# Kernel tuning notes

Measured on AMD Instinct MI355X. Metric: run time of the kernel, lower is better.

## Reference

```python
import jax, jax.numpy as jnp
import numpy as np

E = 16          # ensemble_size
S = 64          # state_size
A = 32          # action_size
R = 1           # reward_size
I = S + A       # combined input size
HS = 64         # SubModel_state hidden
HR = 32         # SubModel_reward hidden
B = 16384       # batch


def setup_inputs() -> dict:
    key = jax.random.key(0)
    ks = jax.random.split(key, 10)

    def init_lin(k, fan_in, shape):
        bound = 1.0 / np.sqrt(fan_in)
        return jax.random.uniform(k, shape, jnp.float32, -bound, bound)

    return {
        "state": jax.random.normal(ks[0], (B, S), jnp.float32),
        "action": jax.random.normal(ks[1], (B, A), jnp.float32),
        # stacked ensemble state-model weights (torch Linear stores [out,in]; we use [in,out])
        "W1": init_lin(ks[2], I, (E, I, HS)),
        "b1": init_lin(ks[3], I, (E, HS)),
        "W2": init_lin(ks[4], HS, (E, HS, S)),
        "b2": init_lin(ks[5], HS, (E, S)),
        # stacked ensemble reward-model weights
        "rW1": init_lin(ks[6], I, (E, I, HR)),
        "rb1": init_lin(ks[7], I, (E, HR)),
        "rW2": init_lin(ks[8], HR, (E, HR, R)),
        "rb2": init_lin(ks[9], HR, (E, R)),
    }


def reference(state, action, W1, b1, W2, b2, rW1, rb1, rW2, rb2):
    x = jnp.concatenate([state, action], axis=1)  # [B, I]
    # state models: Linear -> ReLU -> Linear, all ensemble members in one batched GEMM
    h = jax.nn.relu(jnp.einsum("bi,eih->ebh", x, W1) + b1[:, None, :])  # [E, B, HS]
    pred_states = jnp.einsum("ebh,ehs->ebs", h, W2) + b2[:, None, :]    # [E, B, S]
    # reward models: Linear -> ReLU -> Linear -> clamp(-100, 200)
    hr = jax.nn.relu(jnp.einsum("bi,eih->ebh", x, rW1) + rb1[:, None, :])  # [E, B, HR]
    pred_rewards = jnp.einsum("ebh,ehr->ebr", hr, rW2) + rb2[:, None, :]   # [E, B, R]
    pred_rewards = jnp.clip(pred_rewards, -100.0, 200.0)
    return (pred_states, pred_rewards)
```

## Files before the change

### kernel.cpp

```cpp
#include <hip/hip_runtime.h>
#include <hip/hip_bf16.h>
#include <cstdint>
#include <cstddef>

#define Bsz 16384
#define Esz 16
#define Ssz 64
#define Asz 32
#define Isz 96
#define HSz 64
#define HRz 32

#define NTM 256
#define CHUNK 512
#define NTILE 8

typedef __attribute__((ext_vector_type(8))) short bf16x8;
typedef __attribute__((ext_vector_type(4))) short short4v;
typedef __attribute__((ext_vector_type(4))) float f32x4;

static __device__ __forceinline__ short f2bf(float f) {
    __hip_bfloat16 b = __float2bfloat16(f);
    return *reinterpret_cast<short*>(&b);
}
static __device__ __forceinline__ float bf2f(short s) {
    union { uint32_t u; float f; } v; v.u = ((uint32_t)(uint16_t)s) << 16; return v.f;
}
static __device__ __forceinline__ bf16x8 pack8(float4 lo, float4 hi) {
    bf16x8 r;
    r[0] = f2bf(lo.x); r[1] = f2bf(lo.y); r[2] = f2bf(lo.z); r[3] = f2bf(lo.w);
    r[4] = f2bf(hi.x); r[5] = f2bf(hi.y); r[6] = f2bf(hi.z); r[7] = f2bf(hi.w);
    return r;
}

__global__ __launch_bounds__(NTM, 2)
void fused_all(const float* __restrict__ state, const float* __restrict__ action,
               const float* __restrict__ W1, const float* __restrict__ b1,
               const float* __restrict__ W2, const float* __restrict__ b2,
               const float* __restrict__ rW1, const float* __restrict__ rb1,
               const float* __restrict__ rW2, const float* __restrict__ rb2,
               float* __restrict__ outS, float* __restrict__ outR)
{
    __shared__ __align__(16) short HT[4][16][68];
    __shared__ __align__(16) float OT[4][16][72];

    const int bid = blockIdx.x;
    const int xcd = bid & 7;
    const int rem = bid >> 3;
    const int e   = rem & (Esz - 1);
    const int c0  = (xcd + 8 * (rem >> 4)) * CHUNK;

    const int w = threadIdx.x >> 6, lane = threadIdx.x & 63;
    const int lr = lane & 15, lg = lane >> 4;

    bf16x8 w1r[4][3], rw1r[2][3], w2r[4][2];
    {
        const float* base = W1 + (size_t)e * Isz * HSz;
        #pragma unroll
        for (int nt = 0; nt < 4; ++nt)
            #pragma unroll
            for (int kk = 0; kk < 3; ++kk) {
                const float* p = base + (kk * 32 + lg * 8) * HSz + nt * 16 + lr;
                bf16x8 r;
                #pragma unroll
                for (int t = 0; t < 8; ++t) r[t] = f2bf(p[t * HSz]);
                w1r[nt][kk] = r;
            }
    }
    {
        const float* base = rW1 + (size_t)e * Isz * HRz;
        #pragma unroll
        for (int nt = 0; nt < 2; ++nt)
            #pragma unroll
            for (int kk = 0; kk < 3; ++kk) {
                const float* p = base + (kk * 32 + lg * 8) * HRz + nt * 16 + lr;
                bf16x8 r;
                #pragma unroll
                for (int t = 0; t < 8; ++t) r[t] = f2bf(p[t * HRz]);
                rw1r[nt][kk] = r;
            }
    }
    {
        const float* base = W2 + (size_t)e * HSz * Ssz;
        #pragma unroll
        for (int nt = 0; nt < 4; ++nt)
            #pragma unroll
            for (int kk = 0; kk < 2; ++kk) {
                const float* p = base + (kk * 32 + lg * 8) * Ssz + nt * 16 + lr;
                bf16x8 r;
                #pragma unroll
                for (int t = 0; t < 8; ++t) r[t] = f2bf(p[t * Ssz]);
                w2r[nt][kk] = r;
            }
    }

    short4v b1p[4], b2p[4], rb1p[2], rw2p[2];
    #pragma unroll
    for (int nt = 0; nt < 4; ++nt) {
        float4 v1 = *(const float4*)&b1[e * HSz + nt * 16 + lg * 4];
        float4 v2 = *(const float4*)&b2[e * Ssz + nt * 16 + lg * 4];
        b1p[nt] = (short4v){ f2bf(v1.x), f2bf(v1.y), f2bf(v1.z), f2bf(v1.w) };
        b2p[nt] = (short4v){ f2bf(v2.x), f2bf(v2.y), f2bf(v2.z), f2bf(v2.w) };
    }
    #pragma unroll
    for (int nt = 0; nt < 2; ++nt) {
        float4 v1 = *(const float4*)&rb1[e * HRz + nt * 16 + lg * 4];
        float4 v2 = *(const float4*)&rW2[e * HRz + nt * 16 + lg * 4];
        rb1p[nt] = (short4v){ f2bf(v1.x), f2bf(v1.y), f2bf(v1.z), f2bf(v1.w) };
        rw2p[nt] = (short4v){ f2bf(v2.x), f2bf(v2.y), f2bf(v2.z), f2bf(v2.w) };
    }
    const float rb2s = rb2[e];

    const int row0 = c0 + w * 16 + lr;
    const float* sbase = state  + (size_t)row0 * Ssz + lg * 8;
    const float* abase = action + (size_t)row0 * Asz + lg * 8;

    float4 xs0 = *(const float4*)(sbase);
    float4 xs1 = *(const float4*)(sbase + 4);
    float4 xs2 = *(const float4*)(sbase + 32);
    float4 xs3 = *(const float4*)(sbase + 36);
    float4 xa0 = *(const float4*)(abase);
    float4 xa1 = *(const float4*)(abase + 4);
    bf16x8 a0 = pack8(xs0, xs1);
    bf16x8 a1 = pack8(xs2, xs3);
    bf16x8 a2 = pack8(xa0, xa1);

    #pragma unroll 1
    for (int t = 0; t < NTILE; ++t) {
        const int tn = (t + 1) & (NTILE - 1);
        const float* sp = sbase + (size_t)tn * 64 * Ssz;
        const float* ap = abase + (size_t)tn * 64 * Asz;
        float4 ns0 = *(const float4*)(sp);
        float4 ns1 = *(const float4*)(sp + 4);
        float4 ns2 = *(const float4*)(sp + 32);
        float4 ns3 = *(const float4*)(sp + 36);
        float4 na0 = *(const float4*)(ap);
        float4 na1 = *(const float4*)(ap + 4);

        f32x4 accS[4];
        #pragma unroll
        for (int nt = 0; nt < 4; ++nt) {
            f32x4 acc = (f32x4){ bf2f(b1p[nt][0]), bf2f(b1p[nt][1]),
                                 bf2f(b1p[nt][2]), bf2f(b1p[nt][3]) };
            acc = __builtin_amdgcn_mfma_f32_16x16x32_bf16(w1r[nt][0], a0, acc, 0, 0, 0);
            acc = __builtin_amdgcn_mfma_f32_16x16x32_bf16(w1r[nt][1], a1, acc, 0, 0, 0);
            acc = __builtin_amdgcn_mfma_f32_16x16x32_bf16(w1r[nt][2], a2, acc, 0, 0, 0);
            accS[nt] = acc;
        }
        f32x4 accR[2];
        #pragma unroll
        for (int nt = 0; nt < 2; ++nt) {
            f32x4 acc = (f32x4){ bf2f(rb1p[nt][0]), bf2f(rb1p[nt][1]),
                                 bf2f(rb1p[nt][2]), bf2f(rb1p[nt][3]) };
            acc = __builtin_amdgcn_mfma_f32_16x16x32_bf16(rw1r[nt][0], a0, acc, 0, 0, 0);
            acc = __builtin_amdgcn_mfma_f32_16x16x32_bf16(rw1r[nt][1], a1, acc, 0, 0, 0);
            acc = __builtin_amdgcn_mfma_f32_16x16x32_bf16(rw1r[nt][2], a2, acc, 0, 0, 0);
            accR[nt] = acc;
        }

        #pragma unroll
        for (int nt = 0; nt < 4; ++nt) {
            short4v p = { f2bf(fmaxf(accS[nt][0], 0.f)),
                          f2bf(fmaxf(accS[nt][1], 0.f)),
                          f2bf(fmaxf(accS[nt][2], 0.f)),
                          f2bf(fmaxf(accS[nt][3], 0.f)) };
            *(short4v*)&HT[w][lr][nt * 16 + lg * 4] = p;
        }

        float rp = 0.f;
        #pragma unroll
        for (int nt = 0; nt < 2; ++nt) {
            rp += fmaxf(accR[nt][0], 0.f) * bf2f(rw2p[nt][0]);
            rp += fmaxf(accR[nt][1], 0.f) * bf2f(rw2p[nt][1]);
            rp += fmaxf(accR[nt][2], 0.f) * bf2f(rw2p[nt][2]);
            rp += fmaxf(accR[nt][3], 0.f) * bf2f(rw2p[nt][3]);
        }
        rp += __shfl_xor(rp, 16);
        rp += __shfl_xor(rp, 32);
        if (lane < 16)
            __builtin_nontemporal_store(fminf(fmaxf(rp + rb2s, -100.f), 200.f),
                                        &outR[(size_t)e * Bsz + row0 + t * 64]);

        bf16x8 h0 = *(const bf16x8*)&HT[w][lr][lg * 8];
        bf16x8 h1 = *(const bf16x8*)&HT[w][lr][32 + lg * 8];
        #pragma unroll
        for (int nt = 0; nt < 4; ++nt) {
            f32x4 acc = (f32x4){ bf2f(b2p[nt][0]), bf2f(b2p[nt][1]),
                                 bf2f(b2p[nt][2]), bf2f(b2p[nt][3]) };
            acc = __builtin_amdgcn_mfma_f32_16x16x32_bf16(w2r[nt][0], h0, acc, 0, 0, 0);
            acc = __builtin_amdgcn_mfma_f32_16x16x32_bf16(w2r[nt][1], h1, acc, 0, 0, 0);
            *(f32x4*)&OT[w][lr][nt * 16 + lg * 4] = acc;
        }
        {
            const size_t obase = ((size_t)e * Bsz + c0 + t * 64 + w * 16) * Ssz;
            #pragma unroll
            for (int q = 0; q < 4; ++q) {
                f32x4 v = *(const f32x4*)&OT[w][4 * q + (lane >> 4)][(lane & 15) * 4];
                __builtin_nontemporal_store(v, (f32x4*)&outS[obase + q * 256 + lane * 4]);
            }
        }

        a0 = pack8(ns0, ns1);
        a1 = pack8(ns2, ns3);
        a2 = pack8(na0, na1);
    }
}

extern "C" void kernel_launch(void* const* d_in, const int* in_sizes, int n_in,
                              void* d_out, int out_size, void* d_ws, size_t ws_size,
                              hipStream_t stream) {
    const float* state  = (const float*)d_in[0];
    const float* action = (const float*)d_in[1];
    const float* W1  = (const float*)d_in[2];
    const float* b1  = (const float*)d_in[3];
    const float* W2  = (const float*)d_in[4];
    const float* b2  = (const float*)d_in[5];
    const float* rW1 = (const float*)d_in[6];
    const float* rb1 = (const float*)d_in[7];
    const float* rW2 = (const float*)d_in[8];
    const float* rb2 = (const float*)d_in[9];

    float* outS = (float*)d_out;
    float* outR = outS + (size_t)Esz * Bsz * Ssz;

    fused_all<<<Esz * (Bsz / CHUNK), NTM, 0, stream>>>(
        state, action, W1, b1, W2, b2, rW1, rb1, rW2, rb2, outS, outR);
}
```

Baseline: 25.61 us.

## Split fused state/reward MLP kernel into two kernels with smaller state chunks

Splits the single fused kernel into a state-model kernel and a separate reward-model kernel. The state kernel halves its chunk size, doubling its grid, and raises launch bounds to three blocks per CU to improve occupancy with fewer live registers. The reward kernel re-reads the inputs and recomputes the bf16 packing on its own. In exchange the kernel adds a second launch and re-reads the state and action inputs, which increases memory traffic.

```diff
diff --git a/kernel.cpp b/kernel.cpp
--- a/kernel.cpp
+++ b/kernel.cpp
@@ -12,8 +12,10 @@
 #define HRz 32
 
 #define NTM 256
-#define CHUNK 512
-#define NTILE 8
+#define SCHUNK 256
+#define SNTILE 4
+#define RCHUNK 512
+#define RNTILE 8
 
 typedef __attribute__((ext_vector_type(8))) short bf16x8;
 typedef __attribute__((ext_vector_type(4))) short short4v;
@@ -33,27 +35,25 @@
     return r;
 }
 
-__global__ __launch_bounds__(NTM, 2)
-void fused_all(const float* __restrict__ state, const float* __restrict__ action,
+__global__ __launch_bounds__(NTM, 3)
+void state_mlp(const float* __restrict__ state, const float* __restrict__ action,
                const float* __restrict__ W1, const float* __restrict__ b1,
                const float* __restrict__ W2, const float* __restrict__ b2,
-               const float* __restrict__ rW1, const float* __restrict__ rb1,
-               const float* __restrict__ rW2, const float* __restrict__ rb2,
-               float* __restrict__ outS, float* __restrict__ outR)
+               float* __restrict__ outS)
 {
     __shared__ __align__(16) short HT[4][16][68];
     __shared__ __align__(16) float OT[4][16][72];
 
     const int bid = blockIdx.x;
     const int xcd = bid & 7;
-    const int rem = bid >> 3;
-    const int e   = rem & (Esz - 1);
-    const int c0  = (xcd + 8 * (rem >> 4)) * CHUNK;
+    const int e   = (bid >> 3) & (Esz - 1);
+    const int chi = bid >> 7;
+    const int c0  = (xcd + 8 * chi) * SCHUNK;
 
     const int w = threadIdx.x >> 6, lane = threadIdx.x & 63;
     const int lr = lane & 15, lg = lane >> 4;
 
-    bf16x8 w1r[4][3], rw1r[2][3], w2r[4][2];
+    bf16x8 w1r[4][3], w2r[4][2];
     {
         const float* base = W1 + (size_t)e * Isz * HSz;
         #pragma unroll
@@ -68,19 +68,6 @@
             }
     }
     {
-        const float* base = rW1 + (size_t)e * Isz * HRz;
-        #pragma unroll
-        for (int nt = 0; nt < 2; ++nt)
-            #pragma unroll
-            for (int kk = 0; kk < 3; ++kk) {
-                const float* p = base + (kk * 32 + lg * 8) * HRz + nt * 16 + lr;
-                bf16x8 r;
-                #pragma unroll
-                for (int t = 0; t < 8; ++t) r[t] = f2bf(p[t * HRz]);
-                rw1r[nt][kk] = r;
-            }
-    }
-    {
         const float* base = W2 + (size_t)e * HSz * Ssz;
         #pragma unroll
         for (int nt = 0; nt < 4; ++nt)
@@ -93,8 +80,7 @@
                 w2r[nt][kk] = r;
             }
     }
-
-    short4v b1p[4], b2p[4], rb1p[2], rw2p[2];
+    short4v b1p[4], b2p[4];
     #pragma unroll
     for (int nt = 0; nt < 4; ++nt) {
         float4 v1 = *(const float4*)&b1[e * HSz + nt * 16 + lg * 4];
@@ -102,14 +88,6 @@
         b1p[nt] = (short4v){ f2bf(v1.x), f2bf(v1.y), f2bf(v1.z), f2bf(v1.w) };
         b2p[nt] = (short4v){ f2bf(v2.x), f2bf(v2.y), f2bf(v2.z), f2bf(v2.w) };
     }
-    #pragma unroll
-    for (int nt = 0; nt < 2; ++nt) {
-        float4 v1 = *(const float4*)&rb1[e * HRz + nt * 16 + lg * 4];
-        float4 v2 = *(const float4*)&rW2[e * HRz + nt * 16 + lg * 4];
-        rb1p[nt] = (short4v){ f2bf(v1.x), f2bf(v1.y), f2bf(v1.z), f2bf(v1.w) };
-        rw2p[nt] = (short4v){ f2bf(v2.x), f2bf(v2.y), f2bf(v2.z), f2bf(v2.w) };
-    }
-    const float rb2s = rb2[e];
 
     const int row0 = c0 + w * 16 + lr;
     const float* sbase = state  + (size_t)row0 * Ssz + lg * 8;
@@ -126,8 +104,8 @@
     bf16x8 a2 = pack8(xa0, xa1);
 
     #pragma unroll 1
-    for (int t = 0; t < NTILE; ++t) {
-        const int tn = (t + 1) & (NTILE - 1);
+    for (int t = 0; t < SNTILE; ++t) {
+        const int tn = (t + 1) & (SNTILE - 1);
         const float* sp = sbase + (size_t)tn * 64 * Ssz;
         const float* ap = abase + (size_t)tn * 64 * Asz;
         float4 ns0 = *(const float4*)(sp);
@@ -147,17 +125,6 @@
             acc = __builtin_amdgcn_mfma_f32_16x16x32_bf16(w1r[nt][2], a2, acc, 0, 0, 0);
             accS[nt] = acc;
         }
-        f32x4 accR[2];
-        #pragma unroll
-        for (int nt = 0; nt < 2; ++nt) {
-            f32x4 acc = (f32x4){ bf2f(rb1p[nt][0]), bf2f(rb1p[nt][1]),
-                                 bf2f(rb1p[nt][2]), bf2f(rb1p[nt][3]) };
-            acc = __builtin_amdgcn_mfma_f32_16x16x32_bf16(rw1r[nt][0], a0, acc, 0, 0, 0);
-            acc = __builtin_amdgcn_mfma_f32_16x16x32_bf16(rw1r[nt][1], a1, acc, 0, 0, 0);
-            acc = __builtin_amdgcn_mfma_f32_16x16x32_bf16(rw1r[nt][2], a2, acc, 0, 0, 0);
-            accR[nt] = acc;
-        }
-
         #pragma unroll
         for (int nt = 0; nt < 4; ++nt) {
             short4v p = { f2bf(fmaxf(accS[nt][0], 0.f)),
@@ -166,21 +133,6 @@
                           f2bf(fmaxf(accS[nt][3], 0.f)) };
             *(short4v*)&HT[w][lr][nt * 16 + lg * 4] = p;
         }
-
-        float rp = 0.f;
-        #pragma unroll
-        for (int nt = 0; nt < 2; ++nt) {
-            rp += fmaxf(accR[nt][0], 0.f) * bf2f(rw2p[nt][0]);
-            rp += fmaxf(accR[nt][1], 0.f) * bf2f(rw2p[nt][1]);
-            rp += fmaxf(accR[nt][2], 0.f) * bf2f(rw2p[nt][2]);
-            rp += fmaxf(accR[nt][3], 0.f) * bf2f(rw2p[nt][3]);
-        }
-        rp += __shfl_xor(rp, 16);
-        rp += __shfl_xor(rp, 32);
-        if (lane < 16)
-            __builtin_nontemporal_store(fminf(fmaxf(rp + rb2s, -100.f), 200.f),
-                                        &outR[(size_t)e * Bsz + row0 + t * 64]);
-
         bf16x8 h0 = *(const bf16x8*)&HT[w][lr][lg * 8];
         bf16x8 h1 = *(const bf16x8*)&HT[w][lr][32 + lg * 8];
         #pragma unroll
@@ -199,10 +151,80 @@
                 __builtin_nontemporal_store(v, (f32x4*)&outS[obase + q * 256 + lane * 4]);
             }
         }
-
         a0 = pack8(ns0, ns1);
         a1 = pack8(ns2, ns3);
         a2 = pack8(na0, na1);
+    }
+}
+
+__global__ __launch_bounds__(NTM, 2)
+void reward_mlp(const float* __restrict__ state, const float* __restrict__ action,
+                const float* __restrict__ rW1, const float* __restrict__ rb1,
+                const float* __restrict__ rW2, const float* __restrict__ rb2,
+                float* __restrict__ outR)
+{
+    const int rbid = blockIdx.x;
+    const int e  = rbid & (Esz - 1);
+    const int c0 = (rbid >> 4) * RCHUNK;
+    const int w = threadIdx.x >> 6, lane = threadIdx.x & 63;
+    const int lr = lane & 15, lg = lane >> 4;
+
+    bf16x8 rw1r[2][3];
+    {
+        const float* base = rW1 + (size_t)e * Isz * HRz;
+        #pragma unroll
+        for (int nt = 0; nt < 2; ++nt)
+            #pragma unroll
+            for (int kk = 0; kk < 3; ++kk) {
+                const float* p = base + (kk * 32 + lg * 8) * HRz + nt * 16 + lr;
+                bf16x8 r;
+                #pragma unroll
+                for (int t = 0; t < 8; ++t) r[t] = f2bf(p[t * HRz]);
+                rw1r[nt][kk] = r;
+            }
+    }
+    float4 rb1v[2], rw2v[2];
+    #pragma unroll
+    for (int nt = 0; nt < 2; ++nt) {
+        rb1v[nt] = *(const float4*)&rb1[e * HRz + nt * 16 + lg * 4];
+        rw2v[nt] = *(const float4*)&rW2[e * HRz + nt * 16 + lg * 4];
+    }
+    const float rb2s = rb2[e];
+
+    const int row0 = c0 + w * 16 + lr;
+    const float* sbase = state  + (size_t)row0 * Ssz + lg * 8;
+    const float* abase = action + (size_t)row0 * Asz + lg * 8;
+
+    #pragma unroll 1
+    for (int t = 0; t < RNTILE; ++t) {
+        const float* sp = sbase + (size_t)t * 64 * Ssz;
+        const float* ap = abase + (size_t)t * 64 * Asz;
+        bf16x8 a0 = pack8(*(const float4*)(sp),      *(const float4*)(sp + 4));
+        bf16x8 a1 = pack8(*(const float4*)(sp + 32), *(const float4*)(sp + 36));
+        bf16x8 a2 = pack8(*(const float4*)(ap),      *(const float4*)(ap + 4));
+
+        f32x4 accR[2];
+        #pragma unroll
+        for (int nt = 0; nt < 2; ++nt) {
+            f32x4 acc = (f32x4){ rb1v[nt].x, rb1v[nt].y, rb1v[nt].z, rb1v[nt].w };
+            acc = __builtin_amdgcn_mfma_f32_16x16x32_bf16(rw1r[nt][0], a0, acc, 0, 0, 0);
+            acc = __builtin_amdgcn_mfma_f32_16x16x32_bf16(rw1r[nt][1], a1, acc, 0, 0, 0);
+            acc = __builtin_amdgcn_mfma_f32_16x16x32_bf16(rw1r[nt][2], a2, acc, 0, 0, 0);
+            accR[nt] = acc;
+        }
+        float rp = 0.f;
+        #pragma unroll
+        for (int nt = 0; nt < 2; ++nt) {
+            rp += fmaxf(accR[nt][0], 0.f) * rw2v[nt].x;
+            rp += fmaxf(accR[nt][1], 0.f) * rw2v[nt].y;
+            rp += fmaxf(accR[nt][2], 0.f) * rw2v[nt].z;
+            rp += fmaxf(accR[nt][3], 0.f) * rw2v[nt].w;
+        }
+        rp += __shfl_xor(rp, 16);
+        rp += __shfl_xor(rp, 32);
+        if (lane < 16)
+            __builtin_nontemporal_store(fminf(fmaxf(rp + rb2s, -100.f), 200.f),
+                                        &outR[(size_t)e * Bsz + row0 + t * 64]);
     }
 }
 
@@ -223,6 +245,8 @@
     float* outS = (float*)d_out;
     float* outR = outS + (size_t)Esz * Bsz * Ssz;
 
-    fused_all<<<Esz * (Bsz / CHUNK), NTM, 0, stream>>>(
-        state, action, W1, b1, W2, b2, rW1, rb1, rW2, rb2, outS, outR);
-}
+    state_mlp<<<Esz * (Bsz / SCHUNK), NTM, 0, stream>>>(
+        state, action, W1, b1, W2, b2, outS);
+    reward_mlp<<<Esz * (Bsz / RCHUNK), NTM, 0, stream>>>(
+        state, action, rW1, rb1, rW2, rb2, outR);
+}
```

Result: slower. 44.57 us (+74.1%).

## Split reward path into separate blocks and distribute state N-tiles across waves

Applied to the files above, without the earlier changes.

Each block now runs either the state model or the reward model. Reward blocks each cover 2048 rows. Inside a state block, each wave owns one 16-column output slice across all 64 rows instead of all columns for its own 16 rows, so per-wave weight registers shrink; the layers now exchange data through shared memory with __syncthreads. This cuts register pressure and the reward work that was duplicated alongside the state GEMMs. In exchange it re-reads the input for the reward path, adds block barriers, and drops the register prefetch of the next tile's inputs.

```diff
diff --git a/kernel.cpp b/kernel.cpp
--- a/kernel.cpp
+++ b/kernel.cpp
@@ -12,8 +12,12 @@
 #define HRz 32
 
 #define NTM 256
-#define CHUNK 512
-#define NTILE 8
+#define NSB 512
+#define SCHUNK 512
+#define SNTILE 8
+#define NRB 128
+#define RCHUNK 2048
+#define RNTILE 32
 
 typedef __attribute__((ext_vector_type(8))) short bf16x8;
 typedef __attribute__((ext_vector_type(4))) short short4v;
@@ -33,7 +37,7 @@
     return r;
 }
 
-__global__ __launch_bounds__(NTM, 2)
+__global__ __launch_bounds__(NTM)
 void fused_all(const float* __restrict__ state, const float* __restrict__ action,
                const float* __restrict__ W1, const float* __restrict__ b1,
                const float* __restrict__ W2, const float* __restrict__ b2,
@@ -41,168 +45,151 @@
                const float* __restrict__ rW2, const float* __restrict__ rb2,
                float* __restrict__ outS, float* __restrict__ outR)
 {
-    __shared__ __align__(16) short HT[4][16][68];
-    __shared__ __align__(16) float OT[4][16][72];
+    __shared__ __align__(16) short HT[64][68];
+    __shared__ __align__(16) float OT[64][72];
 
     const int bid = blockIdx.x;
-    const int xcd = bid & 7;
-    const int rem = bid >> 3;
-    const int e   = rem & (Esz - 1);
-    const int c0  = (xcd + 8 * (rem >> 4)) * CHUNK;
-
-    const int w = threadIdx.x >> 6, lane = threadIdx.x & 63;
+    const int tid = threadIdx.x;
+    const int w = tid >> 6, lane = tid & 63;
     const int lr = lane & 15, lg = lane >> 4;
 
-    bf16x8 w1r[4][3], rw1r[2][3], w2r[4][2];
-    {
-        const float* base = W1 + (size_t)e * Isz * HSz;
-        #pragma unroll
-        for (int nt = 0; nt < 4; ++nt)
+    if (bid < NSB) {
+        const int xcd = bid & 7;
+        const int rem = bid >> 3;
+        const int e   = rem & (Esz - 1);
+        const int c0  = (xcd + 8 * (rem >> 4)) * SCHUNK;
+
+        bf16x8 w1r[3], w2r[2];
+        {
+            const float* base = W1 + (size_t)e * Isz * HSz;
             #pragma unroll
             for (int kk = 0; kk < 3; ++kk) {
-                const float* p = base + (kk * 32 + lg * 8) * HSz + nt * 16 + lr;
+                const float* p = base + (kk * 32 + lg * 8) * HSz + w * 16 + lr;
                 bf16x8 r;
                 #pragma unroll
                 for (int t = 0; t < 8; ++t) r[t] = f2bf(p[t * HSz]);
-                w1r[nt][kk] = r;
-            }
-    }
-    {
-        const float* base = rW1 + (size_t)e * Isz * HRz;
-        #pragma unroll
-        for (int nt = 0; nt < 2; ++nt)
-            #pragma unroll
-            for (int kk = 0; kk < 3; ++kk) {
-                const float* p = base + (kk * 32 + lg * 8) * HRz + nt * 16 + lr;
+                w1r[kk] = r;
+            }
+        }
+        {
+            const float* base = W2 + (size_t)e * HSz * Ssz;
+            #pragma unroll
+            for (int kk = 0; kk < 2; ++kk) {
+                const float* p = base + (kk * 32 + lg * 8) * Ssz + w * 16 + lr;
                 bf16x8 r;
                 #pragma unroll
-                for (int t = 0; t < 8; ++t) r[t] = f2bf(p[t * HRz]);
-                rw1r[nt][kk] = r;
-            }
-    }
-    {
-        const float* base = W2 + (size_t)e * HSz * Ssz;
-        #pragma unroll
-        for (int nt = 0; nt < 4; ++nt)
-            #pragma unroll
-            for (int kk = 0; kk < 2; ++kk) {
-                const float* p = base + (kk * 32 + lg * 8) * Ssz + nt * 16 + lr;
-                bf16x8 r;
-                #pragma unroll
                 for (int t = 0; t < 8; ++t) r[t] = f2bf(p[t * Ssz]);
-                w2r[nt][kk] = r;
-            }
-    }
-
-    short4v b1p[4], b2p[4], rb1p[2], rw2p[2];
-    #pragma unroll
-    for (int nt = 0; nt < 4; ++nt) {
-        float4 v1 = *(const float4*)&b1[e * HSz + nt * 16 + lg * 4];
-        float4 v2 = *(const float4*)&b2[e * Ssz + nt * 16 + lg * 4];
-        b1p[nt] = (short4v){ f2bf(v1.x), f2bf(v1.y), f2bf(v1.z), f2bf(v1.w) };
-        b2p[nt] = (short4v){ f2bf(v2.x), f2bf(v2.y), f2bf(v2.z), f2bf(v2.w) };
-    }
-    #pragma unroll
-    for (int nt = 0; nt < 2; ++nt) {
-        float4 v1 = *(const float4*)&rb1[e * HRz + nt * 16 + lg * 4];
-        float4 v2 = *(const float4*)&rW2[e * HRz + nt * 16 + lg * 4];
-        rb1p[nt] = (short4v){ f2bf(v1.x), f2bf(v1.y), f2bf(v1.z), f2bf(v1.w) };
-        rw2p[nt] = (short4v){ f2bf(v2.x), f2bf(v2.y), f2bf(v2.z), f2bf(v2.w) };
-    }
-    const float rb2s = rb2[e];
-
-    const int row0 = c0 + w * 16 + lr;
-    const float* sbase = state  + (size_t)row0 * Ssz + lg * 8;
-    const float* abase = action + (size_t)row0 * Asz + lg * 8;
-
-    float4 xs0 = *(const float4*)(sbase);
-    float4 xs1 = *(const float4*)(sbase + 4);
-    float4 xs2 = *(const float4*)(sbase + 32);
-    float4 xs3 = *(const float4*)(sbase + 36);
-    float4 xa0 = *(const float4*)(abase);
-    float4 xa1 = *(const float4*)(abase + 4);
-    bf16x8 a0 = pack8(xs0, xs1);
-    bf16x8 a1 = pack8(xs2, xs3);
-    bf16x8 a2 = pack8(xa0, xa1);
-
-    #pragma unroll 1
-    for (int t = 0; t < NTILE; ++t) {
-        const int tn = (t + 1) & (NTILE - 1);
-        const float* sp = sbase + (size_t)tn * 64 * Ssz;
-        const float* ap = abase + (size_t)tn * 64 * Asz;
-        float4 ns0 = *(const float4*)(sp);
-        float4 ns1 = *(const float4*)(sp + 4);
-        float4 ns2 = *(const float4*)(sp + 32);
-        float4 ns3 = *(const float4*)(sp + 36);
-        float4 na0 = *(const float4*)(ap);
-        float4 na1 = *(const float4*)(ap + 4);
-
-        f32x4 accS[4];
-        #pragma unroll
-        for (int nt = 0; nt < 4; ++nt) {
-            f32x4 acc = (f32x4){ bf2f(b1p[nt][0]), bf2f(b1p[nt][1]),
-                                 bf2f(b1p[nt][2]), bf2f(b1p[nt][3]) };
-            acc = __builtin_amdgcn_mfma_f32_16x16x32_bf16(w1r[nt][0], a0, acc, 0, 0, 0);
-            acc = __builtin_amdgcn_mfma_f32_16x16x32_bf16(w1r[nt][1], a1, acc, 0, 0, 0);
-            acc = __builtin_amdgcn_mfma_f32_16x16x32_bf16(w1r[nt][2], a2, acc, 0, 0, 0);
-            accS[nt] = acc;
-        }
-        f32x4 accR[2];
+                w2r[kk] = r;
+            }
+        }
+        short4v b1p, b2p;
+        {
+            float4 v1 = *(const float4*)&b1[e * HSz + w * 16 + lg * 4];
+            float4 v2 = *(const float4*)&b2[e * Ssz + w * 16 + lg * 4];
+            b1p = (short4v){ f2bf(v1.x), f2bf(v1.y), f2bf(v1.z), f2bf(v1.w) };
+            b2p = (short4v){ f2bf(v2.x), f2bf(v2.y), f2bf(v2.z), f2bf(v2.w) };
+        }
+
+        #pragma unroll 1
+        for (int t = 0; t < SNTILE; ++t) {
+            const int rbase = c0 + t * 64;
+
+            #pragma unroll 1
+            for (int mt = 0; mt < 4; ++mt) {
+                const int row = rbase + mt * 16 + lr;
+                const float* sp = state  + (size_t)row * Ssz + lg * 8;
+                const float* ap = action + (size_t)row * Asz + lg * 8;
+                bf16x8 a0 = pack8(*(const float4*)(sp),      *(const float4*)(sp + 4));
+                bf16x8 a1 = pack8(*(const float4*)(sp + 32), *(const float4*)(sp + 36));
+                bf16x8 a2 = pack8(*(const float4*)(ap),      *(const float4*)(ap + 4));
+                f32x4 acc = (f32x4){ bf2f(b1p[0]), bf2f(b1p[1]), bf2f(b1p[2]), bf2f(b1p[3]) };
+                acc = __builtin_amdgcn_mfma_f32_16x16x32_bf16(w1r[0], a0, acc, 0, 0, 0);
+                acc = __builtin_amdgcn_mfma_f32_16x16x32_bf16(w1r[1], a1, acc, 0, 0, 0);
+                acc = __builtin_amdgcn_mfma_f32_16x16x32_bf16(w1r[2], a2, acc, 0, 0, 0);
+                short4v p = { f2bf(fmaxf(acc[0], 0.f)), f2bf(fmaxf(acc[1], 0.f)),
+                              f2bf(fmaxf(acc[2], 0.f)), f2bf(fmaxf(acc[3], 0.f)) };
+                *(short4v*)&HT[mt * 16 + lr][w * 16 + lg * 4] = p;
+            }
+            __syncthreads();
+
+            #pragma unroll 1
+            for (int mt = 0; mt < 4; ++mt) {
+                bf16x8 h0 = *(const bf16x8*)&HT[mt * 16 + lr][lg * 8];
+                bf16x8 h1 = *(const bf16x8*)&HT[mt * 16 + lr][32 + lg * 8];
+                f32x4 acc = (f32x4){ bf2f(b2p[0]), bf2f(b2p[1]), bf2f(b2p[2]), bf2f(b2p[3]) };
+                acc = __builtin_amdgcn_mfma_f32_16x16x32_bf16(w2r[0], h0, acc, 0, 0, 0);
+                acc = __builtin_amdgcn_mfma_f32_16x16x32_bf16(w2r[1], h1, acc, 0, 0, 0);
+                *(f32x4*)&OT[mt * 16 + lr][w * 16 + lg * 4] = acc;
+            }
+            __syncthreads();
+
+            {
+                const size_t obase = ((size_t)e * Bsz + rbase) * Ssz;
+                #pragma unroll
+                for (int q = 0; q < 4; ++q) {
+                    const int f = q * 1024 + tid * 4;
+                    f32x4 v = *(const f32x4*)&OT[f >> 6][f & 63];
+                    __builtin_nontemporal_store(v, (f32x4*)&outS[obase + f]);
+                }
+            }
+        }
+    } else {
+        const int rbid = bid - NSB;
+        const int e  = rbid & (Esz - 1);
+        const int c0 = (rbid >> 4) * RCHUNK;
+
+        bf16x8 rw1r[2][3];
+        {
+            const float* base = rW1 + (size_t)e * Isz * HRz;
+            #pragma unroll
+            for (int nt = 0; nt < 2; ++nt)
+                #pragma unroll
+                for (int kk = 0; kk < 3; ++kk) {
+                    const float* p = base + (kk * 32 + lg * 8) * HRz + nt * 16 + lr;
+                    bf16x8 r;
+                    #pragma unroll
+                    for (int t = 0; t < 8; ++t) r[t] = f2bf(p[t * HRz]);
+                    rw1r[nt][kk] = r;
+                }
+        }
+        short4v rb1p[2], rw2p[2];
         #pragma unroll
         for (int nt = 0; nt < 2; ++nt) {
-            f32x4 acc = (f32x4){ bf2f(rb1p[nt][0]), bf2f(rb1p[nt][1]),
-                                 bf2f(rb1p[nt][2]), bf2f(rb1p[nt][3]) };
-            acc = __builtin_amdgcn_mfma_f32_16x16x32_bf16(rw1r[nt][0], a0, acc, 0, 0, 0);
-            acc = __builtin_amdgcn_mfma_f32_16x16x32_bf16(rw1r[nt][1], a1, acc, 0, 0, 0);
-            acc = __builtin_amdgcn_mfma_f32_16x16x32_bf16(rw1r[nt][2], a2, acc, 0, 0, 0);
-            accR[nt] = acc;
-        }
-
-        #pragma unroll
-        for (int nt = 0; nt < 4; ++nt) {
-            short4v p = { f2bf(fmaxf(accS[nt][0], 0.f)),
-                          f2bf(fmaxf(accS[nt][1], 0.f)),
-                          f2bf(fmaxf(accS[nt][2], 0.f)),
-                          f2bf(fmaxf(accS[nt][3], 0.f)) };
-            *(short4v*)&HT[w][lr][nt * 16 + lg * 4] = p;
-        }
-
-        float rp = 0.f;
-        #pragma unroll
-        for (int nt = 0; nt < 2; ++nt) {
-            rp += fmaxf(accR[nt][0], 0.f) * bf2f(rw2p[nt][0]);
-            rp += fmaxf(accR[nt][1], 0.f) * bf2f(rw2p[nt][1]);
-            rp += fmaxf(accR[nt][2], 0.f) * bf2f(rw2p[nt][2]);
-            rp += fmaxf(accR[nt][3], 0.f) * bf2f(rw2p[nt][3]);
-        }
-        rp += __shfl_xor(rp, 16);
-        rp += __shfl_xor(rp, 32);
-        if (lane < 16)
-            __builtin_nontemporal_store(fminf(fmaxf(rp + rb2s, -100.f), 200.f),
-                                        &outR[(size_t)e * Bsz + row0 + t * 64]);
-
-        bf16x8 h0 = *(const bf16x8*)&HT[w][lr][lg * 8];
-        bf16x8 h1 = *(const bf16x8*)&HT[w][lr][32 + lg * 8];
-        #pragma unroll
-        for (int nt = 0; nt < 4; ++nt) {
-            f32x4 acc = (f32x4){ bf2f(b2p[nt][0]), bf2f(b2p[nt][1]),
-                                 bf2f(b2p[nt][2]), bf2f(b2p[nt][3]) };
-            acc = __builtin_amdgcn_mfma_f32_16x16x32_bf16(w2r[nt][0], h0, acc, 0, 0, 0);
-            acc = __builtin_amdgcn_mfma_f32_16x16x32_bf16(w2r[nt][1], h1, acc, 0, 0, 0);
-            *(f32x4*)&OT[w][lr][nt * 16 + lg * 4] = acc;
-        }
-        {
-            const size_t obase = ((size_t)e * Bsz + c0 + t * 64 + w * 16) * Ssz;
-            #pragma unroll
-            for (int q = 0; q < 4; ++q) {
-                f32x4 v = *(const f32x4*)&OT[w][4 * q + (lane >> 4)][(lane & 15) * 4];
-                __builtin_nontemporal_store(v, (f32x4*)&outS[obase + q * 256 + lane * 4]);
-            }
-        }
-
-        a0 = pack8(ns0, ns1);
-        a1 = pack8(ns2, ns3);
-        a2 = pack8(na0, na1);
+            float4 v1 = *(const float4*)&rb1[e * HRz + nt * 16 + lg * 4];
+            float4 v2 = *(const float4*)&rW2[e * HRz + nt * 16 + lg * 4];
+            rb1p[nt] = (short4v){ f2bf(v1.x), f2bf(v1.y), f2bf(v1.z), f2bf(v1.w) };
+            rw2p[nt] = (short4v){ f2bf(v2.x), f2bf(v2.y), f2bf(v2.z), f2bf(v2.w) };
+        }
+        const float rb2s = rb2[e];
+
+        #pragma unroll 1
+        for (int t = 0; t < RNTILE; ++t) {
+            const int row = c0 + t * 64 + w * 16 + lr;
+            const float* sp = state  + (size_t)row * Ssz + lg * 8;
+            const float* ap = action + (size_t)row * Asz + lg * 8;
+            bf16x8 a0 = pack8(*(const float4*)(sp),      *(const float4*)(sp + 4));
+            bf16x8 a1 = pack8(*(const float4*)(sp + 32), *(const float4*)(sp + 36));
+            bf16x8 a2 = pack8(*(const float4*)(ap),      *(const float4*)(ap + 4));
+
+            float rp = 0.f;
+            #pragma unroll
+            for (int nt = 0; nt < 2; ++nt) {
+                f32x4 acc = (f32x4){ bf2f(rb1p[nt][0]), bf2f(rb1p[nt][1]),
+                                     bf2f(rb1p[nt][2]), bf2f(rb1p[nt][3]) };
+                acc = __builtin_amdgcn_mfma_f32_16x16x32_bf16(rw1r[nt][0], a0, acc, 0, 0, 0);
+                acc = __builtin_amdgcn_mfma_f32_16x16x32_bf16(rw1r[nt][1], a1, acc, 0, 0, 0);
+                acc = __builtin_amdgcn_mfma_f32_16x16x32_bf16(rw1r[nt][2], a2, acc, 0, 0, 0);
+                rp += fmaxf(acc[0], 0.f) * bf2f(rw2p[nt][0]);
+                rp += fmaxf(acc[1], 0.f) * bf2f(rw2p[nt][1]);
+                rp += fmaxf(acc[2], 0.f) * bf2f(rw2p[nt][2]);
+                rp += fmaxf(acc[3], 0.f) * bf2f(rw2p[nt][3]);
+            }
+            rp += __shfl_xor(rp, 16);
+            rp += __shfl_xor(rp, 32);
+            if (lane < 16)
+                __builtin_nontemporal_store(fminf(fmaxf(rp + rb2s, -100.f), 200.f),
+                                            &outR[(size_t)e * Bsz + row]);
+        }
     }
 }
 
@@ -223,6 +210,6 @@
     float* outS = (float*)d_out;
     float* outR = outS + (size_t)Esz * Bsz * Ssz;
 
-    fused_all<<<Esz * (Bsz / CHUNK), NTM, 0, stream>>>(
+    fused_all<<<NSB + NRB, NTM, 0, stream>>>(
         state, action, W1, b1, W2, b2, rW1, rb1, rW2, rb2, outS, outR);
 }
```

Result: slower. 73.20 us (+185.9%).
